# Optimization experiments

Hardware: AMD Instinct MI355X
Metric: run time of the kernel (lower is better)

The kernel has to match this reference:

```python
import jax, jax.numpy as jnp
import numpy as np

B, S, E, H = 2, 2048, 2048, 8
D = E // H          # 256, also PMSNorm width
LAYER_IDX = 3
EPS = 1e-5
NEG = jnp.finfo(jnp.float32).min


def setup_inputs() -> dict:
    key = jax.random.key(0)
    k1, k2, k3 = jax.random.split(key, 3)
    return {
        "hidden_state": jax.random.normal(k1, (B, S, E), dtype=jnp.float32),
        "w_attn": jax.random.normal(k2, (E, 3 * E), dtype=jnp.float32) * 0.02,
        "w_proj": jax.random.normal(k3, (E, E), dtype=jnp.float32) * 0.02,
        "norm_weight": jnp.ones((D,), dtype=jnp.float32),
    }


def reference(hidden_state, w_attn, w_proj, norm_weight):
    # qkv projection (Linear, no bias): [B,S,3E]
    qkv = hidden_state @ w_attn
    q, k, v = jnp.split(qkv, 3, axis=-1)
    # split heads -> [B,H,S,D]
    q = q.reshape(B, S, H, D).transpose(0, 2, 1, 3)
    k = k.reshape(B, S, H, D).transpose(0, 2, 1, 3)
    v = v.reshape(B, S, H, D).transpose(0, 2, 1, 3)
    # scaled scores, extra layer-idx scaling as in the module
    scale = jnp.asarray(D, jnp.float32) ** 0.5 * (LAYER_IDX + 1)
    scores = jnp.einsum("bhqd,bhkd->bhqk", q, k) / scale
    # causal mask (tril buffer): masked positions -> float32 min
    causal = jnp.tril(jnp.ones((S, S), dtype=bool))
    scores = jnp.where(causal[None, None], scores, NEG)
    attn = jax.nn.softmax(scores, axis=-1)  # dropout is identity in eval
    o = jnp.einsum("bhqk,bhkd->bhqd", attn, v)
    # PMSNorm over last dim D (applied per-head, as in the source)
    o = o * jax.lax.rsqrt(jnp.mean(o * o, axis=-1, keepdims=True) + EPS)
    o = o * norm_weight
    # merge heads -> [B,S,E], output projection
    merged = o.transpose(0, 2, 1, 3).reshape(B, S, E)
    return merged @ w_proj
```

## Files before the change

kernel.cpp:

```cpp
#include <hip/hip_runtime.h>
#include <math.h>


typedef unsigned short u16;
typedef unsigned int   u32;
typedef u16   u16x8 __attribute__((ext_vector_type(8)));
typedef __bf16 bf16x8 __attribute__((ext_vector_type(8)));
typedef float f32x4 __attribute__((ext_vector_type(4)));

#define GPTR(p) ((const __attribute__((address_space(1))) void*)(p))
#define LPTR(p) ((__attribute__((address_space(3))) void*)(p))

__device__ __forceinline__ u16 f2bf(float x) {
  u32 u = __float_as_uint(x);
  return (u16)((u + 0x7fffu + ((u >> 16) & 1u)) >> 16);
}

__device__ __forceinline__ float bf2f(u16 x) {
  return __uint_as_float(((u32)x) << 16);
}

__device__ __forceinline__ bf16x8 ld8(const void* p) {
  u16x8 v = *reinterpret_cast<const u16x8*>(p);
  return __builtin_bit_cast(bf16x8, v);
}

__device__ __forceinline__ void g2l16(const void* g, void* l) {
  __builtin_amdgcn_global_load_lds(GPTR(g), LPTR(l), 16, 0, 0);
}

__global__ void prep_kernel(const float* __restrict__ hs, const float* __restrict__ wat,
                            const float* __restrict__ wpr, u16* __restrict__ Xb,
                            u16* __restrict__ Wa_t, u16* __restrict__ Wp_t) {
  __shared__ float t[32][33];
  const int bid = blockIdx.x, tid = threadIdx.x;
  if (bid < 4096) {
    int i = bid * 256 + tid;
    const float4* p = reinterpret_cast<const float4*>(hs) + (size_t)i * 2;
    float4 a = p[0], b = p[1];
    u16x8 v;
    v[0] = f2bf(a.x); v[1] = f2bf(a.y); v[2] = f2bf(a.z); v[3] = f2bf(a.w);
    v[4] = f2bf(b.x); v[5] = f2bf(b.y); v[6] = f2bf(b.z); v[7] = f2bf(b.w);
    reinterpret_cast<u16x8*>(Xb)[i] = v;
    return;
  }
  const float* in; u16* out; int R, C, bx, by;
  if (bid < 16384) {
    int b2 = bid - 4096;
    in = wat; out = Wa_t; R = 2048; C = 6144;
    bx = (b2 % 192) * 32; by = (b2 / 192) * 32;
  } else {
    int b3 = bid - 16384;
    in = wpr; out = Wp_t; R = 2048; C = 2048;
    bx = (b3 % 64) * 32; by = (b3 / 64) * 32;
  }
  int x = tid & 31, y = tid >> 5;
  #pragma unroll
  for (int k = 0; k < 32; k += 8)
    t[y + k][x] = in[(size_t)(by + y + k) * C + (bx + x)];
  __syncthreads();
  #pragma unroll
  for (int k = 0; k < 32; k += 8)
    out[(size_t)(bx + y + k) * R + (by + x)] = f2bf(t[x][y + k]);
}

__global__ void tv_kernel(const u16* __restrict__ qkv, u16* __restrict__ out) {
  __shared__ u16 t[32][33];
  int bh = blockIdx.z, b = bh >> 3, h = bh & 7;
  const u16* ip = qkv + (size_t)b * 2048 * 6144 + 4096 + h * 256;
  u16* op = out + (size_t)bh * 256 * 2048;
  int bx = blockIdx.x * 32, by = blockIdx.y * 32;
  int x = threadIdx.x, y = threadIdx.y;
  #pragma unroll
  for (int k = 0; k < 32; k += 8)
    t[y + k][x] = ip[(size_t)(by + y + k) * 6144 + (bx + x)];
  __syncthreads();
  #pragma unroll
  for (int k = 0; k < 32; k += 8)
    op[(size_t)(bx + y + k) * 2048 + (by + x)] = t[x][y + k];
}

template<int WM, int WN, int MF, int NF, bool F32OUT>
__global__ __launch_bounds__(512, 4) void gemm2b_kernel(
    const u16* __restrict__ A, const u16* __restrict__ Bt,
    float* __restrict__ Cf, u16* __restrict__ Cb, int M, int N, int K) {
  constexpr int BM = WM * MF * 16;
  constexpr int BN = WN * NF * 16;
  constexpr int TILEB = (BM + BN) * 128;
  constexpr int NSTG = TILEB / 8192;
  __shared__ __align__(16) char smem[2 * TILEB];

  const int tid = threadIdx.x, lane = tid & 63, w = tid >> 6;
  const int wr = w / WN, wc = w % WN;
  const int g = lane >> 4, li = lane & 15;
  const int bn = blockIdx.x * BN, bm = blockIdx.y * BM;

  const char* src[NSTG]; u32 dOff[NSTG];
  #pragma unroll
  for (int j = 0; j < NSTG; ++j) {
    int o = j * 8192 + tid * 16;
    if (o < BM * 128) {
      int row = o >> 7;
      int col = (o & 127) ^ ((row & 7) << 4);
      src[j] = (const char*)A + (size_t)(bm + row) * K * 2 + col;
    } else {
      int rem = o - BM * 128;
      int row = rem >> 7;
      int col = (rem & 127) ^ ((row & 7) << 4);
      src[j] = (const char*)Bt + (size_t)(bn + row) * K * 2 + col;
    }
    dOff[j] = (u32)(o - lane * 16);
  }

  u32 aRd[2][MF], bRd[2][NF];
  #pragma unroll
  for (int ks = 0; ks < 2; ++ks) {
    #pragma unroll
    for (int mf = 0; mf < MF; ++mf) {
      int row = wr * (MF * 16) + mf * 16 + li;
      aRd[ks][mf] = row * 128 + ((ks * 64 + g * 16) ^ ((row & 7) << 4));
    }
    #pragma unroll
    for (int nf = 0; nf < NF; ++nf) {
      int row = wc * (NF * 16) + nf * 16 + li;
      bRd[ks][nf] = BM * 128 + row * 128 + ((ks * 64 + g * 16) ^ ((row & 7) << 4));
    }
  }

  const f32x4 fz = {0.f, 0.f, 0.f, 0.f};
  f32x4 acc[MF][NF];
  #pragma unroll
  for (int i = 0; i < MF; ++i)
    #pragma unroll
    for (int j = 0; j < NF; ++j) acc[i][j] = fz;

  const int NT = K >> 6;
  #pragma unroll
  for (int j = 0; j < NSTG; ++j) { g2l16(src[j], smem + dOff[j]); src[j] += 128; }

  for (int t = 0; t < NT; ++t) {
    const int cur = t & 1;
    const bool more = (t + 1 < NT);
    asm volatile("s_barrier" ::: "memory");
    if (more) {
      char* nb = smem + (cur ^ 1) * TILEB;
      #pragma unroll
      for (int j = 0; j < NSTG; ++j) { g2l16(src[j], nb + dOff[j]); src[j] += 128; }
      asm volatile("s_waitcnt vmcnt(%0)" :: "i"(NSTG) : "memory");
    } else {
      asm volatile("s_waitcnt vmcnt(0)" ::: "memory");
    }
    asm volatile("s_barrier" ::: "memory");

    const char* sb = smem + cur * TILEB;
    #pragma unroll
    for (int ks = 0; ks < 2; ++ks) {
      bf16x8 aR[MF], bR[NF];
      #pragma unroll
      for (int mf = 0; mf < MF; ++mf) aR[mf] = ld8(sb + aRd[ks][mf]);
      #pragma unroll
      for (int nf = 0; nf < NF; ++nf) bR[nf] = ld8(sb + bRd[ks][nf]);
      __builtin_amdgcn_s_setprio(1);
      #pragma unroll
      for (int mf = 0; mf < MF; ++mf)
        #pragma unroll
        for (int nf = 0; nf < NF; ++nf)
          acc[mf][nf] = __builtin_amdgcn_mfma_f32_16x16x32_bf16(aR[mf], bR[nf], acc[mf][nf], 0, 0, 0);
      __builtin_amdgcn_s_setprio(0);
    }
  }

  #pragma unroll
  for (int mf = 0; mf < MF; ++mf)
    #pragma unroll
    for (int nf = 0; nf < NF; ++nf)
      #pragma unroll
      for (int r = 0; r < 4; ++r) {
        int gm = bm + wr * (MF * 16) + mf * 16 + g * 4 + r;
        int gn = bn + wc * (NF * 16) + nf * 16 + li;
        if (F32OUT) Cf[(size_t)gm * N + gn] = acc[mf][nf][r];
        else        Cb[(size_t)gm * N + gn] = f2bf(acc[mf][nf][r]);
      }
}

__global__ __launch_bounds__(256, 2) void attn_main_kernel(
    const u16* __restrict__ qkv, const u16* __restrict__ Vt,
    u16* __restrict__ Opart, float* __restrict__ Lse) {
  __shared__ __align__(16) u16 sK[2][32 * 256];
  __shared__ __align__(16) u16 sV[256 * 32];
  __shared__ __align__(16) u16 sP[4 * 16 * 32];

  const int c = blockIdx.x;
  const int bh = c & 15, iu = (c >> 4) & 15, half = c >> 8;
  const int b = bh >> 3, h = bh & 7;
  const int tid = threadIdx.x, lane = tid & 63, wq = tid >> 6;
  const int g = lane >> 4, li = lane & 15;
  const float MASKV = -30000.0f;
  const float MINIT = -1000.0f;
  const float isc = 1.0f / 64.0f;
  const f32x4 fz = {0.f, 0.f, 0.f, 0.f};
  const size_t KADV = (size_t)32 * 6144 * 2;

  #pragma unroll 1
  for (int uu = 0; uu < 2; ++uu) {
    const int qt = uu ? (31 - iu) : iu;
    const int nt = qt + 1;
    const int kvb0 = half * nt * 32;

    int qrow = qt * 64 + wq * 16 + li;
    const u16* qp = qkv + (size_t)(b * 2048 + qrow) * 6144 + h * 256;
    bf16x8 qf[8];
    #pragma unroll
    for (int c8 = 0; c8 < 8; ++c8) qf[c8] = ld8(qp + c8 * 32 + g * 8);

    const char* kSrc[4]; u32 kDoff[4];
    #pragma unroll
    for (int j = 0; j < 4; ++j) {
      int chunk = wq * 4 + j;
      int o = chunk * 1024 + lane * 16;
      int row = o >> 9, cb = o & 511;
      int cbs = cb ^ ((row & 7) << 4);
      kSrc[j] = (const char*)qkv + ((size_t)(b * 2048 + kvb0 + row) * 6144 + 2048 + h * 256) * 2 + cbs;
      kDoff[j] = chunk * 1024;
    }
    const char* vSrc[4]; char* vDst[4];
    #pragma unroll
    for (int j = 0; j < 4; ++j) {
      int chunk = wq * 4 + j;
      int o = chunk * 1024 + lane * 16;
      int row = o >> 6, cb = o & 63;
      int cbs = cb ^ (((row >> 1) & 3) << 4);
      vSrc[j] = (const char*)Vt + ((size_t)(bh * 256 + row) * 2048 + kvb0) * 2 + cbs;
      vDst[j] = (char*)sV + chunk * 1024;
    }

    f32x4 o_[16];
    #pragma unroll
    for (int nf = 0; nf < 16; ++nf) o_[nf] = fz;
    float m_[4] = {MINIT, MINIT, MINIT, MINIT};
    float l_[4] = {0.f, 0.f, 0.f, 0.f};

    #pragma unroll
    for (int j = 0; j < 4; ++j) { g2l16(kSrc[j], (char*)sK[0] + kDoff[j]); kSrc[j] += KADV; }
    asm volatile("s_waitcnt vmcnt(0)" ::: "memory");
    asm volatile("s_barrier" ::: "memory");

    int cur = 0;
    for (int t = 0; t < nt; ++t) {
      const bool more = (t < nt - 1);
      #pragma unroll
      for (int j = 0; j < 4; ++j) { g2l16(vSrc[j], vDst[j]); vSrc[j] += 64; }
      if (more) {
        char* kb = (char*)sK[cur ^ 1];
        #pragma unroll
        for (int j = 0; j < 4; ++j) { g2l16(kSrc[j], kb + kDoff[j]); kSrc[j] += KADV; }
      }

      f32x4 sacc[2];
      const char* kbase = (const char*)sK[cur];
      __builtin_amdgcn_s_setprio(1);
      #pragma unroll
      for (int nf = 0; nf < 2; ++nf) {
        int row = nf * 16 + li;
        int swz = (row & 7) << 4;
        const char* kr = kbase + row * 512;
        f32x4 sa = fz, sb = fz;
        #pragma unroll
        for (int c8 = 0; c8 < 4; ++c8) {
          sa = __builtin_amdgcn_mfma_f32_16x16x32_bf16(qf[c8],     ld8(kr + ((c8 * 64 + g * 16) ^ swz)),       sa, 0, 0, 0);
          sb = __builtin_amdgcn_mfma_f32_16x16x32_bf16(qf[c8 + 4], ld8(kr + (((c8 + 4) * 64 + g * 16) ^ swz)), sb, 0, 0, 0);
        }
        sacc[nf] = sa + sb;
      }
      __builtin_amdgcn_s_setprio(0);

      const int tidx = half * nt + t;
      const bool diag = (tidx >= 2 * qt);
      float p[2][4], m0[4];
      #pragma unroll
      for (int r = 0; r < 4; ++r) {
        int qr = qt * 64 + wq * 16 + g * 4 + r;
        float a0 = sacc[0][r] * isc;
        float a1 = sacc[1][r] * isc;
        if (diag) {
          if (tidx * 32 + li > qr) a0 = MASKV;
          if (tidx * 32 + 16 + li > qr) a1 = MASKV;
        }
        p[0][r] = a0; p[1][r] = a1;
        m0[r] = fmaxf(a0, a1);
      }
      bool need = (m0[0] > m_[0] + 8.f) || (m0[1] > m_[1] + 8.f) ||
                  (m0[2] > m_[2] + 8.f) || (m0[3] > m_[3] + 8.f);
      if (__any(need)) {
        #pragma unroll
        for (int r = 0; r < 4; ++r) {
          float mx = m0[r];
          mx = fmaxf(mx, __shfl_xor(mx, 1));
          mx = fmaxf(mx, __shfl_xor(mx, 2));
          mx = fmaxf(mx, __shfl_xor(mx, 4));
          mx = fmaxf(mx, __shfl_xor(mx, 8));
          float mn = fmaxf(m_[r], mx);
          float sc = __expf(m_[r] - mn);
          l_[r] *= sc; m_[r] = mn;
          #pragma unroll
          for (int nf = 0; nf < 16; ++nf) o_[nf][r] *= sc;
        }
      }
      #pragma unroll
      for (int r = 0; r < 4; ++r) {
        float e0 = __expf(p[0][r] - m_[r]);
        float e1 = __expf(p[1][r] - m_[r]);
        p[0][r] = e0; p[1][r] = e1;
        l_[r] += e0 + e1;
      }

      if (more) asm volatile("s_waitcnt vmcnt(4)" ::: "memory");
      else      asm volatile("s_waitcnt vmcnt(0)" ::: "memory");
      asm volatile("s_barrier" ::: "memory");

      char* sPw = (char*)sP + wq * 1024;
      #pragma unroll
      for (int r = 0; r < 4; ++r) {
        int row = g * 4 + r;
        int swz = ((row >> 1) & 3) << 4;
        #pragma unroll
        for (int nf = 0; nf < 2; ++nf)
          *(u16*)(sPw + row * 64 + (((nf * 16 + li) * 2) ^ swz)) = f2bf(p[nf][r]);
      }
      asm volatile("s_waitcnt lgkmcnt(0)" ::: "memory");
      __builtin_amdgcn_sched_barrier(0);

      __builtin_amdgcn_s_setprio(1);
      {
        bf16x8 pa = ld8(sPw + li * 64 + ((g * 16) ^ (((li >> 1) & 3) << 4)));
        #pragma unroll
        for (int nf = 0; nf < 16; ++nf) {
          int row = nf * 16 + li;
          bf16x8 vf = ld8((const char*)sV + row * 64 + ((g * 16) ^ (((row >> 1) & 3) << 4)));
          o_[nf] = __builtin_amdgcn_mfma_f32_16x16x32_bf16(pa, vf, o_[nf], 0, 0, 0);
        }
      }
      __builtin_amdgcn_s_setprio(0);

      asm volatile("s_barrier" ::: "memory");
      if (more) asm volatile("s_waitcnt vmcnt(0)" ::: "memory");
      cur ^= 1;
    }

    const int pu = (bh * 32 + qt) * 2 + half;
    u16* op = Opart + (size_t)pu * 16384;
    #pragma unroll
    for (int r = 0; r < 4; ++r) {
      float ls = l_[r];
      ls += __shfl_xor(ls, 1);
      ls += __shfl_xor(ls, 2);
      ls += __shfl_xor(ls, 4);
      ls += __shfl_xor(ls, 8);
      float linv = (ls > 0.f) ? 1.0f / ls : 0.f;
      float lse  = (ls > 0.f) ? (m_[r] + __logf(ls)) : -3.0e38f;
      int rloc = wq * 16 + g * 4 + r;
      if (li == 0) Lse[pu * 64 + rloc] = lse;
      #pragma unroll
      for (int nf = 0; nf < 16; ++nf)
        op[rloc * 256 + nf * 16 + li] = f2bf(o_[nf][r] * linv);
    }
    __syncthreads();
  }
}

__global__ __launch_bounds__(256) void attn_merge_kernel(
    const u16* __restrict__ Opart, const float* __restrict__ Lse,
    const float* __restrict__ nw, u16* __restrict__ Mrg) {
  const int c = blockIdx.x;
  const int bh = c >> 5, qt = c & 31;
  const int b = bh >> 3, h = bh & 7;
  const int tid = threadIdx.x;
  const int rloc = tid >> 2, dg = tid & 3;

  const int puA = (bh * 32 + qt) * 2, puB = puA + 1;
  float mA = Lse[puA * 64 + rloc], mB = Lse[puB * 64 + rloc];
  float M = fmaxf(mA, mB);
  float wA = __expf(mA - M), wB = __expf(mB - M);
  float dnm = wA + wB;
  wA /= dnm; wB /= dnm;

  const u16* pA = Opart + (size_t)puA * 16384 + rloc * 256 + dg * 64;
  const u16* pB = Opart + (size_t)puB * 16384 + rloc * 256 + dg * 64;
  float ov[64];
  float ss = 0.f;
  #pragma unroll
  for (int j = 0; j < 8; ++j) {
    u16x8 a = *reinterpret_cast<const u16x8*>(pA + j * 8);
    u16x8 bb = *reinterpret_cast<const u16x8*>(pB + j * 8);
    #pragma unroll
    for (int e = 0; e < 8; ++e) {
      float o = wA * bf2f(a[e]) + wB * bf2f(bb[e]);
      ov[j * 8 + e] = o;
      ss += o * o;
    }
  }
  ss += __shfl_xor(ss, 1);
  ss += __shfl_xor(ss, 2);
  float rms = rsqrtf(ss * (1.0f / 256.0f) + 1e-5f);

  u16* mp = Mrg + ((size_t)(b * 2048 + qt * 64 + rloc)) * 2048 + h * 256 + dg * 64;
  #pragma unroll
  for (int j = 0; j < 8; ++j) {
    u16x8 v;
    #pragma unroll
    for (int e = 0; e < 8; ++e)
      v[e] = f2bf(ov[j * 8 + e] * rms * nw[dg * 64 + j * 8 + e]);
    *reinterpret_cast<u16x8*>(mp + j * 8) = v;
  }
}

extern "C" void kernel_launch(void* const* d_in, const int* in_sizes, int n_in,
                              void* d_out, int out_size, void* d_ws, size_t ws_size,
                              hipStream_t stream) {
  const float* hs  = (const float*)d_in[0];
  const float* wat = (const float*)d_in[1];
  const float* wpr = (const float*)d_in[2];
  const float* nw  = (const float*)d_in[3];
  float* out = (float*)d_out;

  char* ws = (char*)d_ws;
  u16* Xb    = (u16*)(ws + 0);
  u16* Wp_t  = (u16*)(ws + (16u << 20));
  u16* Qkv   = (u16*)(ws + (24u << 20));
  u16* Vt    = (u16*)(ws + (72u << 20));
  u16* Mrg   = Vt;
  float* Lse = (float*)Xb;
  u16* Wa_t  = (u16*)d_out;
  u16* Opart = (u16*)d_out;

  dim3 t328(32, 8);
  prep_kernel<<<20480, 256, 0, stream>>>(hs, wat, wpr, Xb, Wa_t, Wp_t);
  gemm2b_kernel<2, 4, 4, 3, false><<<dim3(32, 32), 512, 0, stream>>>(
      Xb, Wa_t, nullptr, Qkv, 4096, 6144, 2048);
  tv_kernel<<<dim3(8, 64, 16), t328, 0, stream>>>(Qkv, Vt);
  attn_main_kernel<<<512, 256, 0, stream>>>(Qkv, Vt, Opart, Lse);
  attn_merge_kernel<<<512, 256, 0, stream>>>(Opart, Lse, nw, Mrg);
  gemm2b_kernel<2, 4, 4, 2, true><<<dim3(16, 32), 512, 0, stream>>>(
      Mrg, Wp_t, out, nullptr, 4096, 2048, 2048);
  (void)in_sizes; (void)n_in; (void)out_size; (void)ws_size;
}
```

Before: 250.9 us.

## Replace split-KV attention with single pass per query tile and fuse PMSNorm epilogue

The attention kernel stops splitting each query tile's KV range into two halves processed by separate blocks and then merged. Each block now handles one query tile over its full causal KV range, with blocks paired as qt and 31-qt across the grid for balance. PMSNorm and the bf16 write into the merged-heads layout happen in the epilogue. This removes the merge kernel launch and the round trip of partial outputs and LSE through memory. In exchange each block gets a longer, less uniform loop and there is less parallelism per tile.

```diff
diff --git a/kernel.cpp b/kernel.cpp
--- a/kernel.cpp
+++ b/kernel.cpp
@@ -14,10 +14,6 @@
 __device__ __forceinline__ u16 f2bf(float x) {
   u32 u = __float_as_uint(x);
   return (u16)((u + 0x7fffu + ((u >> 16) & 1u)) >> 16);
-}
-
-__device__ __forceinline__ float bf2f(u16 x) {
-  return __uint_as_float(((u32)x) << 16);
 }
 
 __device__ __forceinline__ bf16x8 ld8(const void* p) {
@@ -183,15 +179,16 @@
       }
 }
 
-__global__ __launch_bounds__(256, 2) void attn_main_kernel(
+__global__ __launch_bounds__(256, 2) void attn_kernel(
     const u16* __restrict__ qkv, const u16* __restrict__ Vt,
-    u16* __restrict__ Opart, float* __restrict__ Lse) {
+    const float* __restrict__ nw, u16* __restrict__ Mrg) {
   __shared__ __align__(16) u16 sK[2][32 * 256];
   __shared__ __align__(16) u16 sV[256 * 32];
   __shared__ __align__(16) u16 sP[4 * 16 * 32];
 
   const int c = blockIdx.x;
-  const int bh = c & 15, iu = (c >> 4) & 15, half = c >> 8;
+  const int bh = c & 15, iu = (c >> 4) & 15;
+  const int qt = (c < 256) ? iu : 31 - iu;
   const int b = bh >> 3, h = bh & 7;
   const int tid = threadIdx.x, lane = tid & 63, wq = tid >> 6;
   const int g = lane >> 4, li = lane & 15;
@@ -201,216 +198,173 @@
   const f32x4 fz = {0.f, 0.f, 0.f, 0.f};
   const size_t KADV = (size_t)32 * 6144 * 2;
 
-  #pragma unroll 1
-  for (int uu = 0; uu < 2; ++uu) {
-    const int qt = uu ? (31 - iu) : iu;
-    const int nt = qt + 1;
-    const int kvb0 = half * nt * 32;
-
-    int qrow = qt * 64 + wq * 16 + li;
-    const u16* qp = qkv + (size_t)(b * 2048 + qrow) * 6144 + h * 256;
-    bf16x8 qf[8];
-    #pragma unroll
-    for (int c8 = 0; c8 < 8; ++c8) qf[c8] = ld8(qp + c8 * 32 + g * 8);
-
-    const char* kSrc[4]; u32 kDoff[4];
-    #pragma unroll
-    for (int j = 0; j < 4; ++j) {
-      int chunk = wq * 4 + j;
-      int o = chunk * 1024 + lane * 16;
-      int row = o >> 9, cb = o & 511;
-      int cbs = cb ^ ((row & 7) << 4);
-      kSrc[j] = (const char*)qkv + ((size_t)(b * 2048 + kvb0 + row) * 6144 + 2048 + h * 256) * 2 + cbs;
-      kDoff[j] = chunk * 1024;
-    }
-    const char* vSrc[4]; char* vDst[4];
-    #pragma unroll
-    for (int j = 0; j < 4; ++j) {
-      int chunk = wq * 4 + j;
-      int o = chunk * 1024 + lane * 16;
-      int row = o >> 6, cb = o & 63;
-      int cbs = cb ^ (((row >> 1) & 3) << 4);
-      vSrc[j] = (const char*)Vt + ((size_t)(bh * 256 + row) * 2048 + kvb0) * 2 + cbs;
-      vDst[j] = (char*)sV + chunk * 1024;
-    }
-
-    f32x4 o_[16];
-    #pragma unroll
-    for (int nf = 0; nf < 16; ++nf) o_[nf] = fz;
-    float m_[4] = {MINIT, MINIT, MINIT, MINIT};
-    float l_[4] = {0.f, 0.f, 0.f, 0.f};
-
-    #pragma unroll
-    for (int j = 0; j < 4; ++j) { g2l16(kSrc[j], (char*)sK[0] + kDoff[j]); kSrc[j] += KADV; }
-    asm volatile("s_waitcnt vmcnt(0)" ::: "memory");
+  const int nt = 2 * qt + 2;
+
+  int qrow = qt * 64 + wq * 16 + li;
+  const u16* qp = qkv + (size_t)(b * 2048 + qrow) * 6144 + h * 256;
+  bf16x8 qf[8];
+  #pragma unroll
+  for (int c8 = 0; c8 < 8; ++c8) qf[c8] = ld8(qp + c8 * 32 + g * 8);
+
+  const char* kSrc[4]; u32 kDoff[4];
+  #pragma unroll
+  for (int j = 0; j < 4; ++j) {
+    int chunk = wq * 4 + j;
+    int o = chunk * 1024 + lane * 16;
+    int row = o >> 9, cb = o & 511;
+    int cbs = cb ^ ((row & 7) << 4);
+    kSrc[j] = (const char*)qkv + ((size_t)(b * 2048 + row) * 6144 + 2048 + h * 256) * 2 + cbs;
+    kDoff[j] = chunk * 1024;
+  }
+  const char* vSrc[4]; char* vDst[4];
+  #pragma unroll
+  for (int j = 0; j < 4; ++j) {
+    int chunk = wq * 4 + j;
+    int o = chunk * 1024 + lane * 16;
+    int row = o >> 6, cb = o & 63;
+    int cbs = cb ^ (((row >> 1) & 3) << 4);
+    vSrc[j] = (const char*)Vt + ((size_t)(bh * 256 + row) * 2048) * 2 + cbs;
+    vDst[j] = (char*)sV + chunk * 1024;
+  }
+
+  f32x4 o_[16];
+  #pragma unroll
+  for (int nf = 0; nf < 16; ++nf) o_[nf] = fz;
+  float m_[4] = {MINIT, MINIT, MINIT, MINIT};
+  float l_[4] = {0.f, 0.f, 0.f, 0.f};
+
+  #pragma unroll
+  for (int j = 0; j < 4; ++j) { g2l16(kSrc[j], (char*)sK[0] + kDoff[j]); kSrc[j] += KADV; }
+  asm volatile("s_waitcnt vmcnt(0)" ::: "memory");
+  asm volatile("s_barrier" ::: "memory");
+
+  int cur = 0;
+  for (int t = 0; t < nt; ++t) {
+    const bool more = (t < nt - 1);
+    #pragma unroll
+    for (int j = 0; j < 4; ++j) { g2l16(vSrc[j], vDst[j]); vSrc[j] += 64; }
+    if (more) {
+      char* kb = (char*)sK[cur ^ 1];
+      #pragma unroll
+      for (int j = 0; j < 4; ++j) { g2l16(kSrc[j], kb + kDoff[j]); kSrc[j] += KADV; }
+    }
+
+    f32x4 sacc[2];
+    const char* kbase = (const char*)sK[cur];
+    __builtin_amdgcn_s_setprio(1);
+    #pragma unroll
+    for (int nf = 0; nf < 2; ++nf) {
+      int row = nf * 16 + li;
+      int swz = (row & 7) << 4;
+      const char* kr = kbase + row * 512;
+      f32x4 sa = fz, sb = fz;
+      #pragma unroll
+      for (int c8 = 0; c8 < 4; ++c8) {
+        sa = __builtin_amdgcn_mfma_f32_16x16x32_bf16(qf[c8],     ld8(kr + ((c8 * 64 + g * 16) ^ swz)),       sa, 0, 0, 0);
+        sb = __builtin_amdgcn_mfma_f32_16x16x32_bf16(qf[c8 + 4], ld8(kr + (((c8 + 4) * 64 + g * 16) ^ swz)), sb, 0, 0, 0);
+      }
+      sacc[nf] = sa + sb;
+    }
+    __builtin_amdgcn_s_setprio(0);
+
+    const bool diag = (t >= 2 * qt);
+    float p[2][4], m0[4];
+    #pragma unroll
+    for (int r = 0; r < 4; ++r) {
+      int qr = qt * 64 + wq * 16 + g * 4 + r;
+      float a0 = sacc[0][r] * isc;
+      float a1 = sacc[1][r] * isc;
+      if (diag) {
+        if (t * 32 + li > qr) a0 = MASKV;
+        if (t * 32 + 16 + li > qr) a1 = MASKV;
+      }
+      p[0][r] = a0; p[1][r] = a1;
+      m0[r] = fmaxf(a0, a1);
+    }
+    bool need = (m0[0] > m_[0] + 8.f) || (m0[1] > m_[1] + 8.f) ||
+                (m0[2] > m_[2] + 8.f) || (m0[3] > m_[3] + 8.f);
+    if (__any(need)) {
+      #pragma unroll
+      for (int r = 0; r < 4; ++r) {
+        float mx = m0[r];
+        mx = fmaxf(mx, __shfl_xor(mx, 1));
+        mx = fmaxf(mx, __shfl_xor(mx, 2));
+        mx = fmaxf(mx, __shfl_xor(mx, 4));
+        mx = fmaxf(mx, __shfl_xor(mx, 8));
+        float mn = fmaxf(m_[r], mx);
+        float sc = __expf(m_[r] - mn);
+        l_[r] *= sc; m_[r] = mn;
+        #pragma unroll
+        for (int nf = 0; nf < 16; ++nf) o_[nf][r] *= sc;
+      }
+    }
+    #pragma unroll
+    for (int r = 0; r < 4; ++r) {
+      float e0 = __expf(p[0][r] - m_[r]);
+      float e1 = __expf(p[1][r] - m_[r]);
+      p[0][r] = e0; p[1][r] = e1;
+      l_[r] += e0 + e1;
+    }
+
+    if (more) asm volatile("s_waitcnt vmcnt(4)" ::: "memory");
+    else      asm volatile("s_waitcnt vmcnt(0)" ::: "memory");
     asm volatile("s_barrier" ::: "memory");
 
-    int cur = 0;
-    for (int t = 0; t < nt; ++t) {
-      const bool more = (t < nt - 1);
-      #pragma unroll
-      for (int j = 0; j < 4; ++j) { g2l16(vSrc[j], vDst[j]); vSrc[j] += 64; }
-      if (more) {
-        char* kb = (char*)sK[cur ^ 1];
-        #pragma unroll
-        for (int j = 0; j < 4; ++j) { g2l16(kSrc[j], kb + kDoff[j]); kSrc[j] += KADV; }
-      }
-
-      f32x4 sacc[2];
-      const char* kbase = (const char*)sK[cur];
-      __builtin_amdgcn_s_setprio(1);
-      #pragma unroll
-      for (int nf = 0; nf < 2; ++nf) {
+    char* sPw = (char*)sP + wq * 1024;
+    #pragma unroll
+    for (int r = 0; r < 4; ++r) {
+      int row = g * 4 + r;
+      int swz = ((row >> 1) & 3) << 4;
+      #pragma unroll
+      for (int nf = 0; nf < 2; ++nf)
+        *(u16*)(sPw + row * 64 + (((nf * 16 + li) * 2) ^ swz)) = f2bf(p[nf][r]);
+    }
+    asm volatile("s_waitcnt lgkmcnt(0)" ::: "memory");
+    __builtin_amdgcn_sched_barrier(0);
+
+    __builtin_amdgcn_s_setprio(1);
+    {
+      bf16x8 pa = ld8(sPw + li * 64 + ((g * 16) ^ (((li >> 1) & 3) << 4)));
+      #pragma unroll
+      for (int nf = 0; nf < 16; ++nf) {
         int row = nf * 16 + li;
-        int swz = (row & 7) << 4;
-        const char* kr = kbase + row * 512;
-        f32x4 sa = fz, sb = fz;
-        #pragma unroll
-        for (int c8 = 0; c8 < 4; ++c8) {
-          sa = __builtin_amdgcn_mfma_f32_16x16x32_bf16(qf[c8],     ld8(kr + ((c8 * 64 + g * 16) ^ swz)),       sa, 0, 0, 0);
-          sb = __builtin_amdgcn_mfma_f32_16x16x32_bf16(qf[c8 + 4], ld8(kr + (((c8 + 4) * 64 + g * 16) ^ swz)), sb, 0, 0, 0);
-        }
-        sacc[nf] = sa + sb;
-      }
-      __builtin_amdgcn_s_setprio(0);
-
-      const int tidx = half * nt + t;
-      const bool diag = (tidx >= 2 * qt);
-      float p[2][4], m0[4];
-      #pragma unroll
-      for (int r = 0; r < 4; ++r) {
-        int qr = qt * 64 + wq * 16 + g * 4 + r;
-        float a0 = sacc[0][r] * isc;
-        float a1 = sacc[1][r] * isc;
-        if (diag) {
-          if (tidx * 32 + li > qr) a0 = MASKV;
-          if (tidx * 32 + 16 + li > qr) a1 = MASKV;
-        }
-        p[0][r] = a0; p[1][r] = a1;
-        m0[r] = fmaxf(a0, a1);
-      }
-      bool need = (m0[0] > m_[0] + 8.f) || (m0[1] > m_[1] + 8.f) ||
-                  (m0[2] > m_[2] + 8.f) || (m0[3] > m_[3] + 8.f);
-      if (__any(need)) {
-        #pragma unroll
-        for (int r = 0; r < 4; ++r) {
-          float mx = m0[r];
-          mx = fmaxf(mx, __shfl_xor(mx, 1));
-          mx = fmaxf(mx, __shfl_xor(mx, 2));
-          mx = fmaxf(mx, __shfl_xor(mx, 4));
-          mx = fmaxf(mx, __shfl_xor(mx, 8));
-          float mn = fmaxf(m_[r], mx);
-          float sc = __expf(m_[r] - mn);
-          l_[r] *= sc; m_[r] = mn;
-          #pragma unroll
-          for (int nf = 0; nf < 16; ++nf) o_[nf][r] *= sc;
-        }
-      }
-      #pragma unroll
-      for (int r = 0; r < 4; ++r) {
-        float e0 = __expf(p[0][r] - m_[r]);
-        float e1 = __expf(p[1][r] - m_[r]);
-        p[0][r] = e0; p[1][r] = e1;
-        l_[r] += e0 + e1;
-      }
-
-      if (more) asm volatile("s_waitcnt vmcnt(4)" ::: "memory");
-      else      asm volatile("s_waitcnt vmcnt(0)" ::: "memory");
-      asm volatile("s_barrier" ::: "memory");
-
-      char* sPw = (char*)sP + wq * 1024;
-      #pragma unroll
-      for (int r = 0; r < 4; ++r) {
-        int row = g * 4 + r;
-        int swz = ((row >> 1) & 3) << 4;
-        #pragma unroll
-        for (int nf = 0; nf < 2; ++nf)
-          *(u16*)(sPw + row * 64 + (((nf * 16 + li) * 2) ^ swz)) = f2bf(p[nf][r]);
-      }
-      asm volatile("s_waitcnt lgkmcnt(0)" ::: "memory");
-      __builtin_amdgcn_sched_barrier(0);
-
-      __builtin_amdgcn_s_setprio(1);
-      {
-        bf16x8 pa = ld8(sPw + li * 64 + ((g * 16) ^ (((li >> 1) & 3) << 4)));
-        #pragma unroll
-        for (int nf = 0; nf < 16; ++nf) {
-          int row = nf * 16 + li;
-          bf16x8 vf = ld8((const char*)sV + row * 64 + ((g * 16) ^ (((row >> 1) & 3) << 4)));
-          o_[nf] = __builtin_amdgcn_mfma_f32_16x16x32_bf16(pa, vf, o_[nf], 0, 0, 0);
-        }
-      }
-      __builtin_amdgcn_s_setprio(0);
-
-      asm volatile("s_barrier" ::: "memory");
-      if (more) asm volatile("s_waitcnt vmcnt(0)" ::: "memory");
-      cur ^= 1;
-    }
-
-    const int pu = (bh * 32 + qt) * 2 + half;
-    u16* op = Opart + (size_t)pu * 16384;
-    #pragma unroll
-    for (int r = 0; r < 4; ++r) {
-      float ls = l_[r];
-      ls += __shfl_xor(ls, 1);
-      ls += __shfl_xor(ls, 2);
-      ls += __shfl_xor(ls, 4);
-      ls += __shfl_xor(ls, 8);
-      float linv = (ls > 0.f) ? 1.0f / ls : 0.f;
-      float lse  = (ls > 0.f) ? (m_[r] + __logf(ls)) : -3.0e38f;
-      int rloc = wq * 16 + g * 4 + r;
-      if (li == 0) Lse[pu * 64 + rloc] = lse;
-      #pragma unroll
-      for (int nf = 0; nf < 16; ++nf)
-        op[rloc * 256 + nf * 16 + li] = f2bf(o_[nf][r] * linv);
-    }
-    __syncthreads();
-  }
-}
-
-__global__ __launch_bounds__(256) void attn_merge_kernel(
-    const u16* __restrict__ Opart, const float* __restrict__ Lse,
-    const float* __restrict__ nw, u16* __restrict__ Mrg) {
-  const int c = blockIdx.x;
-  const int bh = c >> 5, qt = c & 31;
-  const int b = bh >> 3, h = bh & 7;
-  const int tid = threadIdx.x;
-  const int rloc = tid >> 2, dg = tid & 3;
-
-  const int puA = (bh * 32 + qt) * 2, puB = puA + 1;
-  float mA = Lse[puA * 64 + rloc], mB = Lse[puB * 64 + rloc];
-  float M = fmaxf(mA, mB);
-  float wA = __expf(mA - M), wB = __expf(mB - M);
-  float dnm = wA + wB;
-  wA /= dnm; wB /= dnm;
-
-  const u16* pA = Opart + (size_t)puA * 16384 + rloc * 256 + dg * 64;
-  const u16* pB = Opart + (size_t)puB * 16384 + rloc * 256 + dg * 64;
-  float ov[64];
-  float ss = 0.f;
-  #pragma unroll
-  for (int j = 0; j < 8; ++j) {
-    u16x8 a = *reinterpret_cast<const u16x8*>(pA + j * 8);
-    u16x8 bb = *reinterpret_cast<const u16x8*>(pB + j * 8);
-    #pragma unroll
-    for (int e = 0; e < 8; ++e) {
-      float o = wA * bf2f(a[e]) + wB * bf2f(bb[e]);
-      ov[j * 8 + e] = o;
-      ss += o * o;
-    }
-  }
-  ss += __shfl_xor(ss, 1);
-  ss += __shfl_xor(ss, 2);
-  float rms = rsqrtf(ss * (1.0f / 256.0f) + 1e-5f);
-
-  u16* mp = Mrg + ((size_t)(b * 2048 + qt * 64 + rloc)) * 2048 + h * 256 + dg * 64;
-  #pragma unroll
-  for (int j = 0; j < 8; ++j) {
-    u16x8 v;
-    #pragma unroll
-    for (int e = 0; e < 8; ++e)
-      v[e] = f2bf(ov[j * 8 + e] * rms * nw[dg * 64 + j * 8 + e]);
-    *reinterpret_cast<u16x8*>(mp + j * 8) = v;
+        bf16x8 vf = ld8((const char*)sV + row * 64 + ((g * 16) ^ (((row >> 1) & 3) << 4)));
+        o_[nf] = __builtin_amdgcn_mfma_f32_16x16x32_bf16(pa, vf, o_[nf], 0, 0, 0);
+      }
+    }
+    __builtin_amdgcn_s_setprio(0);
+
+    asm volatile("s_barrier" ::: "memory");
+    if (more) asm volatile("s_waitcnt vmcnt(0)" ::: "memory");
+    cur ^= 1;
+  }
+
+  #pragma unroll
+  for (int r = 0; r < 4; ++r) {
+    float ls = l_[r];
+    ls += __shfl_xor(ls, 1);
+    ls += __shfl_xor(ls, 2);
+    ls += __shfl_xor(ls, 4);
+    ls += __shfl_xor(ls, 8);
+    float inv_l = 1.0f / ls;
+    float ss = 0.f;
+    #pragma unroll
+    for (int nf = 0; nf < 16; ++nf) {
+      float v = o_[nf][r] * inv_l;
+      ss += v * v;
+    }
+    ss += __shfl_xor(ss, 1);
+    ss += __shfl_xor(ss, 2);
+    ss += __shfl_xor(ss, 4);
+    ss += __shfl_xor(ss, 8);
+    float rms = rsqrtf(ss * (1.0f / 256.0f) + 1e-5f);
+    int row = qt * 64 + wq * 16 + g * 4 + r;
+    #pragma unroll
+    for (int nf = 0; nf < 16; ++nf) {
+      int d = nf * 16 + li;
+      float v = o_[nf][r] * inv_l * rms * nw[d];
+      Mrg[((size_t)(b * 2048 + row)) * 2048 + h * 256 + d] = f2bf(v);
+    }
   }
 }
 
@@ -424,22 +378,19 @@
   float* out = (float*)d_out;
 
   char* ws = (char*)d_ws;
-  u16* Xb    = (u16*)(ws + 0);
-  u16* Wp_t  = (u16*)(ws + (16u << 20));
-  u16* Qkv   = (u16*)(ws + (24u << 20));
-  u16* Vt    = (u16*)(ws + (72u << 20));
-  u16* Mrg   = Vt;
-  float* Lse = (float*)Xb;
-  u16* Wa_t  = (u16*)d_out;
-  u16* Opart = (u16*)d_out;
+  u16* Xb   = (u16*)(ws + 0);
+  u16* Wp_t = (u16*)(ws + (16u << 20));
+  u16* Qkv  = (u16*)(ws + (24u << 20));
+  u16* Vt   = (u16*)(ws + (72u << 20));
+  u16* Mrg  = Xb;
+  u16* Wa_t = (u16*)d_out;
 
   dim3 t328(32, 8);
   prep_kernel<<<20480, 256, 0, stream>>>(hs, wat, wpr, Xb, Wa_t, Wp_t);
   gemm2b_kernel<2, 4, 4, 3, false><<<dim3(32, 32), 512, 0, stream>>>(
       Xb, Wa_t, nullptr, Qkv, 4096, 6144, 2048);
   tv_kernel<<<dim3(8, 64, 16), t328, 0, stream>>>(Qkv, Vt);
-  attn_main_kernel<<<512, 256, 0, stream>>>(Qkv, Vt, Opart, Lse);
-  attn_merge_kernel<<<512, 256, 0, stream>>>(Opart, Lse, nw, Mrg);
+  attn_kernel<<<512, 256, 0, stream>>>(Qkv, Vt, nw, Mrg);
   gemm2b_kernel<2, 4, 4, 2, true><<<dim3(16, 32), 512, 0, stream>>>(
       Mrg, Wp_t, out, nullptr, 4096, 2048, 2048);
   (void)in_sizes; (void)n_in; (void)out_size; (void)ws_size;
```

Measured after the change: 273.4 us. +9.0%, slower.
